# Kernel tuning notes

Measured on AMD Instinct MI355X. Metric: run time of the kernel, lower is better.

The kernel has to match this reference:

```python
import jax
jax.config.update("jax_enable_x64", True)
import jax.numpy as jnp
import numpy as np

# NTT-friendly stand-in prime for BLS12-377 Fr (residues fit in int64, products in 62 bits)
P = 2013265921          # 15 * 2^27 + 1
GEN = 31                # generator of (Z/P)^*
COSET = 7               # coset shift generator
LOG_DOMAIN = 21
DOMAIN = 1 << LOG_DOMAIN
BATCH = 8


def _pow_table(base, length):
    """numpy int64 table [base^0, ..., base^(length-1)] mod P, built by doubling."""
    t = np.ones(length, dtype=np.int64)
    k = 1
    while k < length:
        mult = pow(int(base), k, P)          # exact python-int exponentiation
        end = min(2 * k, length)
        t[k:end] = (t[:end - k] * mult) % P  # < 2^62, no overflow
        k = end
    return t


def _bitrev(n):
    b = int(n).bit_length() - 1
    idx = np.arange(n, dtype=np.int64)
    rev = np.zeros(n, dtype=np.int64)
    for i in range(b):
        rev |= ((idx >> i) & 1) << (b - 1 - i)
    return rev


def _ntt_core(x, inverse):
    """Iterative radix-2 Cooley-Tukey NTT over rows of x: [batch, n] int64 residues mod P."""
    b, n = x.shape
    logn = n.bit_length() - 1
    root = pow(GEN, (P - 1) // n, P)         # primitive n-th root of unity
    if inverse:
        root = pow(root, P - 2, P)
    wpow = _pow_table(root, n // 2)          # root^j, j < n/2 (host-side, exact)
    x = x[:, jnp.asarray(_bitrev(n))]        # bit-reversal permutation
    for s in range(1, logn + 1):             # structural loop over log2(n) stages
        m = 1 << s
        half = m >> 1
        tw = jnp.asarray(wpow[:: n // m][:half])   # stage twiddles root^{j*n/m}
        xr = x.reshape(b, n // m, m)
        e, o = xr[..., :half], xr[..., half:]
        t = (o * tw) % P                     # butterfly: vectorized over all groups
        x = jnp.concatenate([(e + t) % P, (e - t) % P], axis=-1).reshape(b, n)
    return x


def setup_inputs() -> dict:
    key = jax.random.key(0)
    inp = jax.random.randint(key, (BATCH, DOMAIN), 0, P, dtype=jnp.int64)
    return {"input": inp, "is_intt": 0, "is_coset": 0}


def reference(input, is_intt, is_coset):
    x = jnp.mod(input, P)
    n = x.shape[-1]
    if (not is_intt) and is_coset:
        # coset NTT: multiply element i by COSET^i before the forward transform
        x = (x * jnp.asarray(_pow_table(COSET, n))) % P
    x = _ntt_core(x, inverse=bool(is_intt))
    if is_intt:
        if is_coset:
            # coset INTT: undo the coset shift after the inverse transform
            x = (x * jnp.asarray(_pow_table(pow(COSET, P - 2, P), n))) % P
        n_inv = pow(int(n), P - 2, P)
        x = (x * n_inv) % P                  # scale by n^{-1}
    return x
```

## Files before the change

### kernel.cpp

```cpp
#include <hip/hip_runtime.h>
#include <stdint.h>

typedef unsigned int u32;
typedef unsigned long long u64;

#define MOD_P 2013265921u

#define T_A      0
#define T_B      16384
#define T_W128P  32768
#define T_RP     49152
#define T_CLP    49216
#define T_CHP    65600
#define T_NINV   65728

__device__ __forceinline__ u32 mul64mod(u32 a, u32 b){ return (u32)((u64)a * b % MOD_P); }

__device__ u32 powmod(u32 b, u32 e){
  u32 r = 1;
  while (e){ if (e & 1) r = mul64mod(r, b); b = mul64mod(b, b); e >>= 1; }
  return r;
}

__device__ __forceinline__ u32 shoup_of(u32 v){ return (u32)(((u64)v << 32) / MOD_P); }

__device__ __forceinline__ u32 redP(u32 a){
  u32 b = a - MOD_P;
  return b < a ? b : a;
}

__device__ __forceinline__ u32 mul_shoup(u32 a, uint2 t){
  u32 q = __umulhi(a, t.y);
  u32 r = a * t.x - q * MOD_P;
  return redP(r);
}

__device__ __forceinline__ constexpr int rev4(int m){
  return ((m&1)<<3) | ((m&2)<<1) | ((m&4)>>1) | ((m&8)>>3);
}

__device__ __forceinline__ void bf(u32 &x, u32 &y, uint2 t){
  u32 s = redP(x + y);
  u32 d = x - y + MOD_P;
  x = s; y = mul_shoup(d, t);
}
__device__ __forceinline__ void bf0(u32 &x, u32 &y){
  u32 s = redP(x + y);
  u32 d = x - y + MOD_P;
  x = s; y = d;
}

__device__ __forceinline__ void stages_p1(u32 v[16], int b, const uint2* __restrict__ twl){
  #pragma unroll
  for (int m = 0; m < 8; ++m) bf(v[m], v[m+8], twl[b + 8*m]);
  #pragma unroll
  for (int g = 0; g < 2; ++g)
    #pragma unroll
    for (int m = 0; m < 4; ++m) bf(v[g*8+m], v[g*8+m+4], twl[(b + 8*m) << 1]);
  #pragma unroll
  for (int g = 0; g < 4; ++g)
    #pragma unroll
    for (int m = 0; m < 2; ++m) bf(v[g*4+m], v[g*4+m+2], twl[(b + 8*m) << 2]);
  #pragma unroll
  for (int k = 0; k < 8; ++k) bf(v[2*k], v[2*k+1], twl[b << 3]);
}
__device__ __forceinline__ void stages_p2(u32 v[16], const uint2* __restrict__ twl){
  #pragma unroll
  for (int g = 0; g < 2; ++g)
    #pragma unroll
    for (int m = 0; m < 4; ++m) bf(v[g*8+m], v[g*8+m+4], twl[m << 4]);
  #pragma unroll
  for (int g = 0; g < 4; ++g)
    #pragma unroll
    for (int m = 0; m < 2; ++m) bf(v[g*4+m], v[g*4+m+2], twl[m << 5]);
  #pragma unroll
  for (int k = 0; k < 8; ++k) bf0(v[2*k], v[2*k+1]);
}

__device__ __forceinline__ int cidx(int row, int a){
  return (row << 7) | (a ^ (row >> 2));
}

extern "C" __global__ void k_gen(uint2* __restrict__ tw, const int* __restrict__ f_intt){
  const u32 tid = blockIdx.x * 256 + threadIdx.x;
  const int intt = f_intt[0];
  const u32 MASK = (1u << 21) - 1;
  u32 v; int dst;
  if (tid < 16384){
    u32 e = (tid >> 7) * (tid & 127);
    if (intt) e = ((1u<<21) - e) & MASK;
    v = powmod(31u, 960u * e); dst = T_A + tid;
  } else if (tid < 32768){
    u32 i = tid - 16384;
    u32 e = (((i >> 7) * (i & 127)) << 7) & MASK;
    if (intt) e = ((1u<<21) - e) & MASK;
    v = powmod(31u, 960u * e); dst = T_B + i;
  } else if (tid < 49152){
    u32 i = tid - 32768;
    u32 e = (i << 7) & MASK;
    if (intt) e = ((1u<<21) - e) & MASK;
    v = powmod(31u, 960u * e); dst = T_W128P + i;
  } else if (tid < 65536){
    u32 i = tid - 49152;
    v = intt ? powmod(7u, (MOD_P - 1 - i) % (MOD_P - 1)) : powmod(7u, i);
    dst = T_CLP + i;
  } else if (tid < 65664){
    u32 e = (tid - 65536) << 14;
    v = intt ? powmod(7u, MOD_P - 1 - e) : powmod(7u, e);
    dst = T_CHP + (tid - 65536);
  } else if (tid < 65728){
    u32 e = ((tid - 65664) << 14) & MASK;
    if (intt) e = ((1u<<21) - e) & MASK;
    v = powmod(31u, 960u * e); dst = T_RP + (tid - 65664);
  } else if (tid == 65728){
    v = powmod(1u << 21, MOD_P - 2); dst = T_NINV;
  } else return;
  tw[dst] = make_uint2(v, shoup_of(v));
}

extern "C" __global__ void __launch_bounds__(1024, 8) k_passA(
    const u32* __restrict__ x, u32* __restrict__ y, const uint2* __restrict__ tw,
    const int* __restrict__ f_intt, const int* __restrict__ f_coset)
{
  __shared__ u32 lds[16384];
  const int wg = blockIdx.x;
  const int jb = wg & 127;
  const int batch = wg >> 7;
  const int t = threadIdx.x;
  const u32* xb = x + ((size_t)batch << 21) + (jb << 7);
  u32* yb = y + ((size_t)batch << 21);
  const uint2* twl = tw + T_RP;
  {
    const int q = t & 31, rr = t >> 5;
    #pragma unroll
    for (int i = 0; i < 4; ++i){
      const int ja = rr + 32*i;
      uint4 v4 = *(const uint4*)(xb + ((size_t)ja << 14) + (q << 2));
      u32* d = &lds[(ja << 7) | (q << 2)];
      d[0] = redP(v4.x); d[1] = redP(v4.y); d[2] = redP(v4.z); d[3] = redP(v4.w);
    }
  }
  __syncthreads();
  const int jc = t & 127;
  const int b = __builtin_amdgcn_readfirstlane(t >> 7);
  u32 v[16];
  #pragma unroll
  for (int m = 0; m < 16; ++m) v[m] = lds[((b + 8*m) << 7) | jc];
  if ((f_intt[0] == 0) && (f_coset[0] != 0)){
    uint2 cl = tw[T_CLP + (jb << 7) + jc];
    #pragma unroll
    for (int m = 0; m < 16; ++m){
      v[m] = mul_shoup(v[m], cl);
      v[m] = mul_shoup(v[m], tw[T_CHP + b + 8*m]);
    }
  }
  stages_p1(v, b, twl);
  #pragma unroll
  for (int m = 0; m < 16; ++m) lds[((b + 8*m) << 7) | jc] = v[m];
  __syncthreads();
  #pragma unroll
  for (int m = 0; m < 16; ++m) v[m] = lds[((16*b + m) << 7) | jc];
  stages_p2(v, twl);
  const int rb = ((b&1)<<2) | (b&2) | ((b&4)>>2);
  #pragma unroll
  for (int m = 0; m < 16; ++m){
    const int ka = (rev4(m) << 3) | rb;
    u32 vv = mul_shoup(v[m], tw[T_A + (ka << 7) + jc]);
    vv = mul_shoup(vv, tw[T_W128P + ka * jb]);
    yb[((size_t)ka << 14) + (jb << 7) + jc] = vv;
  }
}

extern "C" __global__ void __launch_bounds__(1024, 8) k_passB(
    u32* __restrict__ y, const uint2* __restrict__ tw)
{
  __shared__ u32 lds[16384];
  const int wg = blockIdx.x;
  const int ka = wg & 127;
  const int batch = wg >> 7;
  const int t = threadIdx.x;
  u32* yb = y + ((size_t)batch << 21) + ((size_t)ka << 14);
  const uint2* twl = tw + T_RP;
  {
    const uint4* s4 = (const uint4*)yb;
    uint4* l4 = (uint4*)lds;
    #pragma unroll
    for (int i = 0; i < 4; ++i) l4[t + 1024*i] = s4[t + 1024*i];
  }
  __syncthreads();
  const int jc = t & 127;
  const int b = __builtin_amdgcn_readfirstlane(t >> 7);
  u32 v[16];
  #pragma unroll
  for (int m = 0; m < 16; ++m) v[m] = lds[((b + 8*m) << 7) | jc];
  stages_p1(v, b, twl);
  #pragma unroll
  for (int m = 0; m < 16; ++m) lds[((b + 8*m) << 7) | jc] = v[m];
  __syncthreads();
  #pragma unroll
  for (int m = 0; m < 16; ++m) v[m] = lds[((16*b + m) << 7) | jc];
  stages_p2(v, twl);
  const int rb = ((b&1)<<2) | (b&2) | ((b&4)>>2);
  #pragma unroll
  for (int m = 0; m < 16; ++m){
    const int kb = (rev4(m) << 3) | rb;
    u32 vv = mul_shoup(v[m], tw[T_B + (kb << 7) + jc]);
    yb[(kb << 7) + jc] = vv;
  }
}

extern "C" __global__ void __launch_bounds__(1024, 8) k_passC(
    u32* __restrict__ y, const uint2* __restrict__ tw,
    const int* __restrict__ f_intt, const int* __restrict__ f_coset)
{
  __shared__ u32 lds[16384];
  const int wg = blockIdx.x;
  const int kb = wg & 127;
  const int batch = wg >> 7;
  u32* yb = y + ((size_t)batch << 21);
  const u32* base = yb + (kb << 7);
  const int t = threadIdx.x;
  {
    const int q = t & 31;
    const int rr = t >> 5;
    #pragma unroll
    for (int i = 0; i < 4; ++i){
      int kaL = rr + 32*i;
      uint4 v4 = *(const uint4*)(base + ((size_t)kaL << 14) + (q << 2));
      lds[cidx(4*q+0, kaL)] = v4.x;
      lds[cidx(4*q+1, kaL)] = v4.y;
      lds[cidx(4*q+2, kaL)] = v4.z;
      lds[cidx(4*q+3, kaL)] = v4.w;
    }
  }
  __syncthreads();
  const int a = t & 127;
  const int b = __builtin_amdgcn_readfirstlane(t >> 7);
  const uint2* twl = tw + T_RP;
  u32 v[16];
  #pragma unroll
  for (int m = 0; m < 16; ++m) v[m] = lds[cidx(b + 8*m, a)];
  stages_p1(v, b, twl);
  #pragma unroll
  for (int m = 0; m < 16; ++m) lds[cidx(b + 8*m, a)] = v[m];
  __syncthreads();
  #pragma unroll
  for (int m = 0; m < 16; ++m) v[m] = lds[cidx(16*b + m, a)];
  stages_p2(v, twl);
  const int rb = ((b&1)<<2) | (b&2) | ((b&4)>>2);
  const int intt = f_intt[0];
  const int coset = f_coset[0];
  #pragma unroll
  for (int m = 0; m < 16; ++m){
    const int kc = (rev4(m) << 3) | rb;
    u32 vv = v[m];
    if (intt){
      vv = mul_shoup(vv, tw[T_NINV]);
      if (coset){
        vv = mul_shoup(vv, tw[T_CLP + (kb << 7) + a]);
        vv = mul_shoup(vv, tw[T_CHP + kc]);
      }
    } else {
      vv = redP(vv);
    }
    __builtin_nontemporal_store(vv, yb + ((size_t)kc << 14) + (kb << 7) + a);
  }
}

extern "C" void kernel_launch(void* const* d_in, const int* in_sizes, int n_in,
                              void* d_out, int out_size, void* d_ws, size_t ws_size,
                              hipStream_t stream)
{
  const u32* x = (const u32*)d_in[0];
  const int* f_intt  = (const int*)d_in[1];
  const int* f_coset = (const int*)d_in[2];
  u32* y   = (u32*)d_out;
  uint2* tw = (uint2*)d_ws;
  const int batch = in_sizes[0] >> 21;
  const int nwg = batch << 7;

  k_gen  <<<257,  256, 0, stream>>>(tw, f_intt);
  k_passA<<<nwg, 1024, 0, stream>>>(x, y, tw, f_intt, f_coset);
  k_passB<<<nwg, 1024, 0, stream>>>(y, tw);
  k_passC<<<nwg, 1024, 0, stream>>>(y, tw, f_intt, f_coset);
}
```

Baseline: 103.3 us.

## Route pass A output through transposed workspace buffer for coalesced pass B

Adds variants of pass A and pass B that go through a separate workspace buffer. Pass A writes its output transposed into the buffer, so pass B can read contiguous 128-element rows with vector loads and write its results straight into the output layout pass C expects. The global loads in passes A and C are also split so all four vector loads are issued before the LDS stores, to overlap memory latency. The new path needs an extra 64 MiB of workspace and falls back to the old kernels if the workspace is too small.

New measurement: 99.73 us. 3.5% less time.

```diff
diff --git a/kernel.cpp b/kernel.cpp
--- a/kernel.cpp
+++ b/kernel.cpp
@@ -118,6 +118,107 @@
   tw[dst] = make_uint2(v, shoup_of(v));
 }
 
+extern "C" __global__ void __launch_bounds__(1024, 8) k_passA_z(
+    const u32* __restrict__ x, u32* __restrict__ z, const uint2* __restrict__ tw,
+    const int* __restrict__ f_intt, const int* __restrict__ f_coset)
+{
+  __shared__ u32 lds[16384];
+  const int wg = blockIdx.x;
+  const int jb = wg & 127;
+  const int batch = wg >> 7;
+  const int t = threadIdx.x;
+  const u32* xb = x + ((size_t)batch << 21) + (jb << 7);
+  u32* zb = z + ((size_t)batch << 21) + (jb << 14);
+  const uint2* twl = tw + T_RP;
+  {
+    const int q = t & 31, rr = t >> 5;
+    uint4 tmp[4];
+    #pragma unroll
+    for (int i = 0; i < 4; ++i)
+      tmp[i] = *(const uint4*)(xb + ((size_t)(rr + 32*i) << 14) + (q << 2));
+    #pragma unroll
+    for (int i = 0; i < 4; ++i){
+      u32* d = &lds[((rr + 32*i) << 7) | (q << 2)];
+      d[0] = redP(tmp[i].x); d[1] = redP(tmp[i].y);
+      d[2] = redP(tmp[i].z); d[3] = redP(tmp[i].w);
+    }
+  }
+  __syncthreads();
+  const int jc = t & 127;
+  const int b = __builtin_amdgcn_readfirstlane(t >> 7);
+  u32 v[16];
+  #pragma unroll
+  for (int m = 0; m < 16; ++m) v[m] = lds[((b + 8*m) << 7) | jc];
+  if ((f_intt[0] == 0) && (f_coset[0] != 0)){
+    uint2 cl = tw[T_CLP + (jb << 7) + jc];
+    #pragma unroll
+    for (int m = 0; m < 16; ++m){
+      v[m] = mul_shoup(v[m], cl);
+      v[m] = mul_shoup(v[m], tw[T_CHP + b + 8*m]);
+    }
+  }
+  stages_p1(v, b, twl);
+  #pragma unroll
+  for (int m = 0; m < 16; ++m) lds[((b + 8*m) << 7) | jc] = v[m];
+  __syncthreads();
+  #pragma unroll
+  for (int m = 0; m < 16; ++m) v[m] = lds[((16*b + m) << 7) | jc];
+  stages_p2(v, twl);
+  const int rb = ((b&1)<<2) | (b&2) | ((b&4)>>2);
+  #pragma unroll
+  for (int m = 0; m < 16; ++m){
+    const int ka = (rev4(m) << 3) | rb;
+    u32 vv = mul_shoup(v[m], tw[T_A + (ka << 7) + jc]);
+    vv = mul_shoup(vv, tw[T_W128P + ka * jb]);
+    zb[(ka << 7) + jc] = vv;
+  }
+}
+
+extern "C" __global__ void __launch_bounds__(1024, 8) k_passB_z(
+    const u32* __restrict__ z, u32* __restrict__ y, const uint2* __restrict__ tw)
+{
+  __shared__ u32 lds[16384];
+  const int wg = blockIdx.x;
+  const int ka = wg & 127;
+  const int batch = wg >> 7;
+  const int t = threadIdx.x;
+  const u32* zb = z + ((size_t)batch << 21) + (ka << 7);
+  u32* yb = y + ((size_t)batch << 21) + ((size_t)ka << 14);
+  const uint2* twl = tw + T_RP;
+  {
+    const int q = t & 31, rr = t >> 5;
+    uint4 tmp[4];
+    #pragma unroll
+    for (int i = 0; i < 4; ++i)
+      tmp[i] = *(const uint4*)(zb + ((size_t)(rr + 32*i) << 14) + (q << 2));
+    #pragma unroll
+    for (int i = 0; i < 4; ++i){
+      u32* d = &lds[((rr + 32*i) << 7) | (q << 2)];
+      d[0] = tmp[i].x; d[1] = tmp[i].y; d[2] = tmp[i].z; d[3] = tmp[i].w;
+    }
+  }
+  __syncthreads();
+  const int jc = t & 127;
+  const int b = __builtin_amdgcn_readfirstlane(t >> 7);
+  u32 v[16];
+  #pragma unroll
+  for (int m = 0; m < 16; ++m) v[m] = lds[((b + 8*m) << 7) | jc];
+  stages_p1(v, b, twl);
+  #pragma unroll
+  for (int m = 0; m < 16; ++m) lds[((b + 8*m) << 7) | jc] = v[m];
+  __syncthreads();
+  #pragma unroll
+  for (int m = 0; m < 16; ++m) v[m] = lds[((16*b + m) << 7) | jc];
+  stages_p2(v, twl);
+  const int rb = ((b&1)<<2) | (b&2) | ((b&4)>>2);
+  #pragma unroll
+  for (int m = 0; m < 16; ++m){
+    const int kb = (rev4(m) << 3) | rb;
+    u32 vv = mul_shoup(v[m], tw[T_B + (kb << 7) + jc]);
+    yb[(kb << 7) + jc] = vv;
+  }
+}
+
 extern "C" __global__ void __launch_bounds__(1024, 8) k_passA(
     const u32* __restrict__ x, u32* __restrict__ y, const uint2* __restrict__ tw,
     const int* __restrict__ f_intt, const int* __restrict__ f_coset)
@@ -132,12 +233,15 @@
   const uint2* twl = tw + T_RP;
   {
     const int q = t & 31, rr = t >> 5;
+    uint4 tmp[4];
+    #pragma unroll
+    for (int i = 0; i < 4; ++i)
+      tmp[i] = *(const uint4*)(xb + ((size_t)(rr + 32*i) << 14) + (q << 2));
     #pragma unroll
     for (int i = 0; i < 4; ++i){
-      const int ja = rr + 32*i;
-      uint4 v4 = *(const uint4*)(xb + ((size_t)ja << 14) + (q << 2));
-      u32* d = &lds[(ja << 7) | (q << 2)];
-      d[0] = redP(v4.x); d[1] = redP(v4.y); d[2] = redP(v4.z); d[3] = redP(v4.w);
+      u32* d = &lds[((rr + 32*i) << 7) | (q << 2)];
+      d[0] = redP(tmp[i].x); d[1] = redP(tmp[i].y);
+      d[2] = redP(tmp[i].z); d[3] = redP(tmp[i].w);
     }
   }
   __syncthreads();
@@ -223,14 +327,17 @@
   {
     const int q = t & 31;
     const int rr = t >> 5;
+    uint4 tmp[4];
+    #pragma unroll
+    for (int i = 0; i < 4; ++i)
+      tmp[i] = *(const uint4*)(base + ((size_t)(rr + 32*i) << 14) + (q << 2));
     #pragma unroll
     for (int i = 0; i < 4; ++i){
       int kaL = rr + 32*i;
-      uint4 v4 = *(const uint4*)(base + ((size_t)kaL << 14) + (q << 2));
-      lds[cidx(4*q+0, kaL)] = v4.x;
-      lds[cidx(4*q+1, kaL)] = v4.y;
-      lds[cidx(4*q+2, kaL)] = v4.z;
-      lds[cidx(4*q+3, kaL)] = v4.w;
+      lds[cidx(4*q+0, kaL)] = tmp[i].x;
+      lds[cidx(4*q+1, kaL)] = tmp[i].y;
+      lds[cidx(4*q+2, kaL)] = tmp[i].z;
+      lds[cidx(4*q+3, kaL)] = tmp[i].w;
     }
   }
   __syncthreads();
@@ -279,8 +386,17 @@
   const int batch = in_sizes[0] >> 21;
   const int nwg = batch << 7;
 
-  k_gen  <<<257,  256, 0, stream>>>(tw, f_intt);
-  k_passA<<<nwg, 1024, 0, stream>>>(x, y, tw, f_intt, f_coset);
-  k_passB<<<nwg, 1024, 0, stream>>>(y, tw);
+  k_gen<<<257, 256, 0, stream>>>(tw, f_intt);
+
+  const size_t zoff = (size_t)1 << 20;
+  const size_t need = zoff + ((size_t)batch << 23);
+  if (ws_size >= need){
+    u32* z = (u32*)((char*)d_ws + zoff);
+    k_passA_z<<<nwg, 1024, 0, stream>>>(x, z, tw, f_intt, f_coset);
+    k_passB_z<<<nwg, 1024, 0, stream>>>(z, y, tw);
+  } else {
+    k_passA<<<nwg, 1024, 0, stream>>>(x, y, tw, f_intt, f_coset);
+    k_passB<<<nwg, 1024, 0, stream>>>(y, tw);
+  }
   k_passC<<<nwg, 1024, 0, stream>>>(y, tw, f_intt, f_coset);
 }
```
